# Optimization experiments

Measured on AMD Instinct MI355X. Metric: run time of the kernel, lower is better.

The kernel has to match this reference:

```python
import jax, jax.numpy as jnp
import numpy as np
from jax import lax

# Model dims (from init_kwargs / mamba_ssm defaults)
D_MODEL = 256
EXPAND = 2
D_INNER = EXPAND * D_MODEL      # 512
D_STATE = 64                     # ssm_rank
DT_RANK = D_MODEL // 16          # 16 (mamba_ssm default ceil(d_model/16))
D_CONV = 4
IMG = 384
PATCH = 16
BATCH = 16
NUM_CLASSES = 10
NBLK = 6                         # sum(depths) = 2+2+2
GRID = IMG // PATCH
NTOK = GRID * GRID + 1           # 577 (patches + cls token)


def setup_inputs() -> dict:
    key = jax.random.key(0)
    ks = iter(jax.random.split(key, 32))
    rn = lambda shape, s=0.02: jax.random.normal(next(ks), shape, jnp.float32) * s
    inp = {}
    inp["x"] = jax.random.normal(next(ks), (BATCH, 3, IMG, IMG), jnp.float32)
    # patch embed conv
    inp["patch_w"] = rn((D_MODEL, 3, PATCH, PATCH), 0.05)
    inp["patch_b"] = jnp.zeros((D_MODEL,), jnp.float32)
    inp["cls_token"] = rn((1, 1, D_MODEL))
    inp["pos_embed"] = rn((1, NTOK, D_MODEL))
    # stacked per-block Mamba params
    inp["norm_w"] = jnp.ones((NBLK, D_MODEL), jnp.float32)
    inp["norm_b"] = jnp.zeros((NBLK, D_MODEL), jnp.float32)
    inp["in_proj_w"] = rn((NBLK, 2 * D_INNER, D_MODEL))
    inp["conv_w"] = rn((NBLK, D_INNER, 1, D_CONV), 0.1)
    inp["conv_b"] = jnp.zeros((NBLK, D_INNER), jnp.float32)
    inp["x_proj_w"] = rn((NBLK, DT_RANK + 2 * D_STATE, D_INNER))
    inp["dt_proj_w"] = rn((NBLK, D_INNER, DT_RANK), 0.1)
    inp["dt_proj_b"] = rn((NBLK, D_INNER), 0.5)
    # S4D-real init: A = -[1..d_state]
    inp["A_log"] = jnp.log(jnp.broadcast_to(
        jnp.arange(1, D_STATE + 1, dtype=jnp.float32), (NBLK, D_INNER, D_STATE)))
    inp["D_ssm"] = jnp.ones((NBLK, D_INNER), jnp.float32)
    inp["out_proj_w"] = rn((NBLK, D_MODEL, D_INNER))
    inp["fnorm_w"] = jnp.ones((D_MODEL,), jnp.float32)
    inp["fnorm_b"] = jnp.zeros((D_MODEL,), jnp.float32)
    inp["head_w"] = rn((NUM_CLASSES, D_MODEL))
    inp["head_b"] = jnp.zeros((NUM_CLASSES,), jnp.float32)
    return inp


def layer_norm(x, w, b, eps=1e-5):
    mu = jnp.mean(x, axis=-1, keepdims=True)
    var = jnp.mean(jnp.square(x - mu), axis=-1, keepdims=True)
    return (x - mu) * lax.rsqrt(var + eps) * w + b


def causal_dwconv(x, w, b):
    # x: (B, di, L), w: (di, 1, K) depthwise; causal left pad K-1
    K = w.shape[-1]
    y = lax.conv_general_dilated(x, w, (1,), [(K - 1, 0)],
                                 dimension_numbers=("NCH", "OIH", "NCH"),
                                 feature_group_count=x.shape[1])
    return y + b[None, :, None]


def selective_scan(u, dt, A, Bm, Cm, Dp):
    # u, dt: (B, L, di); Bm, Cm: (B, L, ds); A: (di, ds); Dp: (di,)
    def step(h, inp):
        dt_t, B_t, C_t, u_t = inp                       # (B,di),(B,ds),(B,ds),(B,di)
        dA = jnp.exp(dt_t[:, :, None] * A)              # (B, di, ds)
        h = dA * h + (dt_t * u_t)[:, :, None] * B_t[:, None, :]
        y = jnp.einsum('bds,bs->bd', h, C_t)
        return h, y
    h0 = jnp.zeros((u.shape[0], A.shape[0], A.shape[1]), u.dtype)
    _, ys = lax.scan(step, h0, (dt.transpose(1, 0, 2), Bm.transpose(1, 0, 2),
                                Cm.transpose(1, 0, 2), u.transpose(1, 0, 2)))
    return ys.transpose(1, 0, 2) + u * Dp


def mamba_block(x, nw, nb, inw, cw, cb, xpw, dtw, dtb, alog, dp, ow):
    res = x
    x = layer_norm(x, nw, nb)
    xz = jnp.einsum('bld,ed->ble', x, inw)              # (B, L, 2*di)
    xi, z = jnp.split(xz, 2, axis=-1)
    xi = causal_dwconv(xi.transpose(0, 2, 1), cw, cb).transpose(0, 2, 1)
    xi = jax.nn.silu(xi)
    dbl = jnp.einsum('bld,ed->ble', xi, xpw)            # (B, L, dt_rank + 2*ds)
    dtr = dbl[..., :DT_RANK]
    Bm = dbl[..., DT_RANK:DT_RANK + D_STATE]
    Cm = dbl[..., DT_RANK + D_STATE:]
    dt = jax.nn.softplus(jnp.einsum('blr,dr->bld', dtr, dtw) + dtb)
    A = -jnp.exp(alog)
    y = selective_scan(xi, dt, A, Bm, Cm, dp)
    y = y * jax.nn.silu(z)
    return res + jnp.einsum('bld,ed->ble', y, ow)


def reference(x, patch_w, patch_b, cls_token, pos_embed,
              norm_w, norm_b, in_proj_w, conv_w, conv_b, x_proj_w,
              dt_proj_w, dt_proj_b, A_log, D_ssm, out_proj_w,
              fnorm_w, fnorm_b, head_w, head_b):
    B = x.shape[0]
    h = lax.conv_general_dilated(x, patch_w, (PATCH, PATCH), 'VALID',
                                 dimension_numbers=("NCHW", "OIHW", "NCHW"))
    h = h + patch_b[None, :, None, None]
    h = h.reshape(B, D_MODEL, -1).transpose(0, 2, 1)    # (B, G*G, D)
    h = jnp.concatenate([jnp.broadcast_to(cls_token, (B, 1, D_MODEL)), h], axis=1)
    h = h + pos_embed
    for i in range(NBLK):
        h = mamba_block(h, norm_w[i], norm_b[i], in_proj_w[i], conv_w[i], conv_b[i],
                        x_proj_w[i], dt_proj_w[i], dt_proj_b[i], A_log[i], D_ssm[i],
                        out_proj_w[i])
    h = layer_norm(h, fnorm_w, fnorm_b)
    return h[:, 0] @ head_w.T + head_b
```

## Files before the change

kernel.cpp:

```cpp
#include <hip/hip_runtime.h>
#include <hip/hip_bf16.h>
#include <cstdint>
#include <cstddef>

#define L_TOK 577
#define DM 256
#define DI 512
#define DS_ 64
#define NROWS (16*577)
#define PROWS (16*576)
#define NCH 37

typedef float f32x4v __attribute__((ext_vector_type(4)));
typedef __bf16 bf16x8 __attribute__((ext_vector_type(8)));

__device__ __forceinline__ float fast_exp2(float x) {
#if __has_builtin(__builtin_amdgcn_exp2f)
    return __builtin_amdgcn_exp2f(x);
#else
    return __expf(x * 0.6931471805599453f);
#endif
}

__global__ __launch_bounds__(256)
void k_gemm(const float* __restrict__ A, int lda,
            const float* __restrict__ B, int ldb,
            float* __restrict__ C, int ldc,
            int M, int N, int K, int beta)
{
    __shared__ char sA[128*64*2];
    __shared__ char sB[128*64*2];
    const int tid  = threadIdx.x;
    const int lane = tid & 63;
    const int wave = tid >> 6;
    const int wr = wave >> 1, wc = wave & 1;
    const int tm = blockIdx.y * 128, tn = blockIdx.x * 128;

    f32x4v acc[4][4];
#pragma unroll
    for (int m = 0; m < 4; ++m)
#pragma unroll
        for (int n = 0; n < 4; ++n) acc[m][n] = (f32x4v){0.f, 0.f, 0.f, 0.f};

    const int nk = K >> 6;
    for (int kt = 0; kt < nk; ++kt) {
        const int k0 = kt << 6;
        __syncthreads();
#pragma unroll
        for (int i = 0; i < 4; ++i) {
            int c = tid + (i << 8);
            int row = c >> 3, slot = c & 7;
            int gr = tm + row; gr = gr < M ? gr : M - 1;
            const float* src = A + (size_t)gr * lda + k0 + (slot << 3);
            float4 lo = *reinterpret_cast<const float4*>(src);
            float4 hi = *reinterpret_cast<const float4*>(src + 4);
            bf16x8 pk;
            pk[0]=(__bf16)lo.x; pk[1]=(__bf16)lo.y; pk[2]=(__bf16)lo.z; pk[3]=(__bf16)lo.w;
            pk[4]=(__bf16)hi.x; pk[5]=(__bf16)hi.y; pk[6]=(__bf16)hi.z; pk[7]=(__bf16)hi.w;
            *reinterpret_cast<bf16x8*>(&sA[(row << 7) + ((slot ^ (row & 7)) << 4)]) = pk;
        }
#pragma unroll
        for (int i = 0; i < 4; ++i) {
            int c = tid + (i << 8);
            int row = c >> 3, slot = c & 7;
            int gr = tn + row; gr = gr < N ? gr : N - 1;
            const float* src = B + (size_t)gr * ldb + k0 + (slot << 3);
            float4 lo = *reinterpret_cast<const float4*>(src);
            float4 hi = *reinterpret_cast<const float4*>(src + 4);
            bf16x8 pk;
            pk[0]=(__bf16)lo.x; pk[1]=(__bf16)lo.y; pk[2]=(__bf16)lo.z; pk[3]=(__bf16)lo.w;
            pk[4]=(__bf16)hi.x; pk[5]=(__bf16)hi.y; pk[6]=(__bf16)hi.z; pk[7]=(__bf16)hi.w;
            *reinterpret_cast<bf16x8*>(&sB[(row << 7) + ((slot ^ (row & 7)) << 4)]) = pk;
        }
        __syncthreads();

        bf16x8 af[4][2], bfr[4][2];
#pragma unroll
        for (int kk = 0; kk < 2; ++kk) {
            int sl = (kk << 2) + (lane >> 4);
#pragma unroll
            for (int m = 0; m < 4; ++m) {
                int row = (wr << 6) + (m << 4) + (lane & 15);
                af[m][kk] = *reinterpret_cast<const bf16x8*>(&sA[(row << 7) + ((sl ^ (row & 7)) << 4)]);
            }
#pragma unroll
            for (int n = 0; n < 4; ++n) {
                int row = (wc << 6) + (n << 4) + (lane & 15);
                bfr[n][kk] = *reinterpret_cast<const bf16x8*>(&sB[(row << 7) + ((sl ^ (row & 7)) << 4)]);
            }
        }
#pragma unroll
        for (int kk = 0; kk < 2; ++kk)
#pragma unroll
            for (int m = 0; m < 4; ++m)
#pragma unroll
                for (int n = 0; n < 4; ++n)
                    acc[m][n] = __builtin_amdgcn_mfma_f32_16x16x32_bf16(af[m][kk], bfr[n][kk], acc[m][n], 0, 0, 0);
    }

#pragma unroll
    for (int m = 0; m < 4; ++m) {
        int grow0 = tm + (wr << 6) + (m << 4) + ((lane >> 4) << 2);
#pragma unroll
        for (int n = 0; n < 4; ++n) {
            int gcol = tn + (wc << 6) + (n << 4) + (lane & 15);
            if (gcol < N) {
#pragma unroll
                for (int j = 0; j < 4; ++j) {
                    int grow = grow0 + j;
                    if (grow < M) {
                        size_t o = (size_t)grow * ldc + gcol;
                        float v = acc[m][n][j];
                        if (beta) v += C[o];
                        C[o] = v;
                    }
                }
            }
        }
    }
}

__global__ __launch_bounds__(256)
void k_im2col(const float* __restrict__ x, float* __restrict__ xcol)
{
    int id = blockIdx.x * 256 + threadIdx.x;
    int kh = id & 15;
    int ci = (id >> 4) % 3;
    int row = id / 48;
    int b = row / 576, p = row % 576;
    int py = p / 24, px = p % 24;
    const float* src = x + ((size_t)(b*3 + ci)*384 + py*16 + kh)*384 + px*16;
    float* dst = xcol + (size_t)row*768 + ci*256 + kh*16;
#pragma unroll
    for (int j = 0; j < 4; ++j)
        *reinterpret_cast<float4*>(dst + j*4) = *reinterpret_cast<const float4*>(src + j*4);
}

__global__ __launch_bounds__(256)
void k_assemble(const float* __restrict__ Ctmp, const float* __restrict__ pb,
                const float* __restrict__ cls, const float* __restrict__ pos,
                float* __restrict__ h_tok)
{
    int i4 = blockIdx.x * 256 + threadIdx.x;
    int c4 = i4 & 63;
    int tok = (i4 >> 6) % 577;
    int b = i4 / (577*64);
    float4 pv = *reinterpret_cast<const float4*>(pos + tok*256 + c4*4);
    float4 r;
    if (tok == 0) {
        float4 cv = *reinterpret_cast<const float4*>(cls + c4*4);
        r.x = cv.x + pv.x; r.y = cv.y + pv.y; r.z = cv.z + pv.z; r.w = cv.w + pv.w;
    } else {
        float4 t = *reinterpret_cast<const float4*>(Ctmp + (size_t)(b*576 + tok - 1)*256 + c4*4);
        float4 bb = *reinterpret_cast<const float4*>(pb + c4*4);
        r.x = t.x + bb.x + pv.x; r.y = t.y + bb.y + pv.y;
        r.z = t.z + bb.z + pv.z; r.w = t.w + bb.w + pv.w;
    }
    *reinterpret_cast<float4*>(h_tok + (size_t)i4*4) = r;
}

__global__ __launch_bounds__(256)
void k_ln(const float* __restrict__ X, const float* __restrict__ w,
          const float* __restrict__ bb, float* __restrict__ O)
{
    int lane = threadIdx.x & 63;
    int row = blockIdx.x * 4 + (threadIdx.x >> 6);
    const float4 v = *reinterpret_cast<const float4*>(X + (size_t)row*256 + lane*4);
    float s1 = v.x + v.y + v.z + v.w;
    float s2 = v.x*v.x + v.y*v.y + v.z*v.z + v.w*v.w;
#pragma unroll
    for (int o2 = 32; o2; o2 >>= 1) { s1 += __shfl_xor(s1, o2); s2 += __shfl_xor(s2, o2); }
    float mu = s1 * (1.f/256.f);
    float var = s2 * (1.f/256.f) - mu*mu;
    float rs = rsqrtf(var + 1e-5f);
    float4 wv = *reinterpret_cast<const float4*>(w + lane*4);
    float4 bv = *reinterpret_cast<const float4*>(bb + lane*4);
    float4 o;
    o.x = (v.x - mu)*rs*wv.x + bv.x;
    o.y = (v.y - mu)*rs*wv.y + bv.y;
    o.z = (v.z - mu)*rs*wv.z + bv.z;
    o.w = (v.w - mu)*rs*wv.w + bv.w;
    *reinterpret_cast<float4*>(O + (size_t)row*256 + lane*4) = o;
}

__global__ __launch_bounds__(256)
void k_conv(const float* __restrict__ xz, const float* __restrict__ cw,
            const float* __restrict__ cb, float* __restrict__ xi)
{
    int gw = blockIdx.x * 4 + (threadIdx.x >> 6);
    int lane = threadIdx.x & 63;
    int tc = gw % 73;
    int eg = (gw / 73) & 7;
    int b  = gw / (73*8);
    int e = eg*64 + lane;
    float4 wv = *reinterpret_cast<const float4*>(cw + e*4);
    float bias = cb[e];
    int t0 = tc * 8;
    float xv[11];
#pragma unroll
    for (int j = 0; j < 11; ++j) {
        int t = t0 - 3 + j;
        xv[j] = (t >= 0 && t < 577) ? xz[(size_t)(b*577 + t)*1024 + e] : 0.f;
    }
#pragma unroll
    for (int j = 0; j < 8; ++j) {
        int t = t0 + j;
        if (t < 577) {
            float a = wv.x*xv[j] + wv.y*xv[j+1] + wv.z*xv[j+2] + wv.w*xv[j+3] + bias;
            float sgm = 1.f / (1.f + __expf(-a));
            xi[(size_t)(b*577 + t)*512 + e] = a * sgm;
        }
    }
}

__global__ __launch_bounds__(256)
void k_dtfuse(const float* __restrict__ dbl, const float* __restrict__ dtw,
              const float* __restrict__ dtb, const float* __restrict__ xi,
              float* __restrict__ tri2)
{
    __shared__ float dtr[16][16];
    const int tid = threadIdx.x;
    const int b    = blockIdx.x / 74;
    const int rr   = blockIdx.x % 74;
    const int tc   = rr >> 1;
    const int e    = ((rr & 1) << 8) + tid;
    const int nj   = (tc == 36) ? 1 : 16;
    {
        int j = tid >> 4, r = tid & 15;
        if (tid < 256 && j < nj)
            dtr[j][r] = dbl[((size_t)(b*577) + tc*16 + j)*144 + r];
    }
    __syncthreads();
    const float* wp = dtw + e*16;
    float4 w0 = *reinterpret_cast<const float4*>(wp);
    float4 w1 = *reinterpret_cast<const float4*>(wp + 4);
    float4 w2 = *reinterpret_cast<const float4*>(wp + 8);
    float4 w3 = *reinterpret_cast<const float4*>(wp + 12);
    float bias = dtb[e];
    float* outp = tri2 + ((size_t)(b*37 + tc)*512 + e)*32;
    for (int j = 0; j < nj; ++j) {
        const float* dr = dtr[j];
        float accv = bias;
        accv += w0.x*dr[0] + w0.y*dr[1] + w0.z*dr[2] + w0.w*dr[3];
        accv += w1.x*dr[4] + w1.y*dr[5] + w1.z*dr[6] + w1.w*dr[7];
        accv += w2.x*dr[8] + w2.y*dr[9] + w2.z*dr[10] + w2.w*dr[11];
        accv += w3.x*dr[12] + w3.y*dr[13] + w3.z*dr[14] + w3.w*dr[15];
        float sp = accv > 20.f ? accv : log1pf(__expf(accv));
        float u = xi[((size_t)(b*577) + tc*16 + j)*512 + e];
        float2 o; o.x = sp; o.y = sp * u;
        *reinterpret_cast<float2*>(outp + j*2) = o;
    }
}

__global__ __launch_bounds__(256, 6)
void k_scan(const float* __restrict__ tri2, const float* __restrict__ dbl,
            const float* __restrict__ A_log, float* __restrict__ y)
{
    __shared__ float tp[4*16*65];
    const int tid  = threadIdx.x;
    const int lane = tid & 63;
    const int wv   = tid >> 6;
    const int bb   = blockIdx.x >> 7;
    const int d    = __builtin_amdgcn_readfirstlane(((blockIdx.x & 127) << 2) + wv);
    const float alog2 = -__expf(A_log[(size_t)d*64 + lane]) * 1.44269504f;
    const float2* trp = reinterpret_cast<const float2*>(tri2)
                      + ((size_t)bb*NCH*512 + d)*16;
    const float* Bb = dbl + (size_t)bb*577*144 + 16 + lane;
    float* yp = y + (size_t)bb*577*512 + d;
    float* tpw = tp + wv*(16*65);
    const int g = lane >> 4, tt = lane & 15;
    float h = 0.f;

    for (int c = 0; c < 36; ++c) {
        const int t0 = c << 4;
        float p[16];
#pragma unroll
        for (int j = 0; j < 16; ++j) {
            float2 tr = trp[(size_t)c*8192 + j];
            float Bv = Bb[(size_t)(t0 + j)*144];
            float Cv = Bb[(size_t)(t0 + j)*144 + 64];
            float dA = fast_exp2(tr.x * alog2);
            h = __builtin_fmaf(dA, h, tr.y * Bv);
            p[j] = h * Cv;
        }
#pragma unroll
        for (int j = 0; j < 16; ++j) tpw[j*65 + lane] = p[j];
        float partial = 0.f;
        {
            const float* rp = tpw + tt*65 + g*16;
#pragma unroll
            for (int k = 0; k < 16; ++k) partial += rp[k];
        }
        partial += __shfl_xor(partial, 16);
        partial += __shfl_xor(partial, 32);
        if (lane < 16) yp[(size_t)(t0 + tt)*512] = partial;
    }
    {
        float2 tr = trp[(size_t)36*8192];
        float Bv = Bb[(size_t)576*144];
        float Cv = Bb[(size_t)576*144 + 64];
        float dA = fast_exp2(tr.x * alog2);
        h = __builtin_fmaf(dA, h, tr.y * Bv);
        float p = h * Cv;
        p += __shfl_xor(p, 32); p += __shfl_xor(p, 16); p += __shfl_xor(p, 8);
        p += __shfl_xor(p, 4);  p += __shfl_xor(p, 2);  p += __shfl_xor(p, 1);
        if (lane == 0) yp[(size_t)576*512] = p;
    }
}

__global__ __launch_bounds__(256)
void k_gate(float* __restrict__ y, const float* __restrict__ xz,
            const float* __restrict__ xi, const float* __restrict__ Dp)
{
    int i4 = blockIdx.x * 256 + threadIdx.x;
    int row = i4 >> 7;
    int c4 = i4 & 127;
    float4 yv = *reinterpret_cast<float4*>(y + (size_t)i4*4);
    float4 uv = *reinterpret_cast<const float4*>(xi + (size_t)i4*4);
    float4 dv = *reinterpret_cast<const float4*>(Dp + c4*4);
    const float4 zv = *reinterpret_cast<const float4*>(xz + (size_t)row*1024 + 512 + c4*4);
    float4 o;
    o.x = (yv.x + uv.x*dv.x) * (zv.x / (1.f + __expf(-zv.x)));
    o.y = (yv.y + uv.y*dv.y) * (zv.y / (1.f + __expf(-zv.y)));
    o.z = (yv.z + uv.z*dv.z) * (zv.z / (1.f + __expf(-zv.z)));
    o.w = (yv.w + uv.w*dv.w) * (zv.w / (1.f + __expf(-zv.w)));
    *reinterpret_cast<float4*>(y + (size_t)i4*4) = o;
}

__global__ __launch_bounds__(256)
void k_head(const float* __restrict__ h_tok, const float* __restrict__ fw,
            const float* __restrict__ fb, const float* __restrict__ hw,
            const float* __restrict__ hb, float* __restrict__ out)
{
    int b = blockIdx.x, tid = threadIdx.x;
    __shared__ float sv[256];
    __shared__ float sr[16];
    float v = h_tok[(size_t)b*577*256 + tid];
    float s1 = v, s2 = v*v;
#pragma unroll
    for (int o2 = 32; o2; o2 >>= 1) { s1 += __shfl_xor(s1, o2); s2 += __shfl_xor(s2, o2); }
    int wave = tid >> 6;
    if ((tid & 63) == 0) { sr[wave] = s1; sr[wave + 8] = s2; }
    __syncthreads();
    float t1 = sr[0] + sr[1] + sr[2] + sr[3];
    float t2 = sr[8] + sr[9] + sr[10] + sr[11];
    float mu = t1 * (1.f/256.f);
    float var = t2 * (1.f/256.f) - mu*mu;
    float rs = rsqrtf(var + 1e-5f);
    sv[tid] = (v - mu)*rs*fw[tid] + fb[tid];
    __syncthreads();
    if (tid < 10) {
        float acc = hb[tid];
        for (int d2 = 0; d2 < 256; ++d2) acc += sv[d2]*hw[tid*256 + d2];
        out[b*10 + tid] = acc;
    }
}

extern "C" void kernel_launch(void* const* d_in, const int* in_sizes, int n_in,
                              void* d_out, int out_size, void* d_ws, size_t ws_size,
                              hipStream_t stream)
{
    const float* x         = (const float*)d_in[0];
    const float* patch_w   = (const float*)d_in[1];
    const float* patch_b   = (const float*)d_in[2];
    const float* cls_tok   = (const float*)d_in[3];
    const float* pos_emb   = (const float*)d_in[4];
    const float* norm_w    = (const float*)d_in[5];
    const float* norm_b    = (const float*)d_in[6];
    const float* in_proj_w = (const float*)d_in[7];
    const float* conv_w    = (const float*)d_in[8];
    const float* conv_b    = (const float*)d_in[9];
    const float* x_proj_w  = (const float*)d_in[10];
    const float* dt_proj_w = (const float*)d_in[11];
    const float* dt_proj_b = (const float*)d_in[12];
    const float* A_log     = (const float*)d_in[13];
    const float* D_ssm     = (const float*)d_in[14];
    const float* out_proj_w= (const float*)d_in[15];
    const float* fnorm_w   = (const float*)d_in[16];
    const float* fnorm_b   = (const float*)d_in[17];
    const float* head_w    = (const float*)d_in[18];
    const float* head_b    = (const float*)d_in[19];
    float* out = (float*)d_out;

    char* ws = (char*)d_ws;
    size_t off = 0;
    auto carve = [&](size_t bytes) -> float* {
        float* p = (float*)(ws + off);
        off += (bytes + 255) & ~(size_t)255;
        return p;
    };
    float* h_tok = carve((size_t)NROWS*DM*4);
    float* xln   = carve((size_t)NROWS*DM*4);
    float* xz    = carve((size_t)NROWS*1024*4);
    float* xi    = carve((size_t)NROWS*DI*4);
    float* dbl   = carve((size_t)NROWS*144*4);
    float* tri2  = carve((size_t)16*NCH*DI*32*4);
    float* yb    = carve((size_t)NROWS*DI*4);
    float* xcol  = xz;
    float* Ctmp  = xi;

    k_im2col<<<1728, 256, 0, stream>>>(x, xcol);
    {
        dim3 g(2, 72);
        k_gemm<<<g, 256, 0, stream>>>(xcol, 768, patch_w, 768, Ctmp, 256, PROWS, 256, 768, 0);
    }
    k_assemble<<<2308, 256, 0, stream>>>(Ctmp, patch_b, cls_tok, pos_emb, h_tok);

    for (int i = 0; i < 6; ++i) {
        k_ln<<<2308, 256, 0, stream>>>(h_tok, norm_w + i*DM, norm_b + i*DM, xln);
        {
            dim3 g(8, 73);
            k_gemm<<<g, 256, 0, stream>>>(xln, DM, in_proj_w + (size_t)i*1024*DM, DM,
                                          xz, 1024, NROWS, 1024, DM, 0);
        }
        k_conv<<<2336, 256, 0, stream>>>(xz, conv_w + (size_t)i*DI*4, conv_b + i*DI, xi);
        {
            dim3 g(2, 73);
            k_gemm<<<g, 256, 0, stream>>>(xi, DI, x_proj_w + (size_t)i*144*DI, DI,
                                          dbl, 144, NROWS, 144, DI, 0);
        }
        k_dtfuse<<<16*NCH*2, 256, 0, stream>>>(dbl, dt_proj_w + (size_t)i*DI*16, dt_proj_b + i*DI,
                                               xi, tri2);
        k_scan<<<2048, 256, 0, stream>>>(tri2, dbl, A_log + (size_t)i*DI*DS_, yb);
        k_gate<<<4616, 256, 0, stream>>>(yb, xz, xi, D_ssm + i*DI);
        {
            dim3 g(2, 73);
            k_gemm<<<g, 256, 0, stream>>>(yb, DI, out_proj_w + (size_t)i*DM*DI, DI,
                                          h_tok, DM, NROWS, DM, DI, 1);
        }
    }
    k_head<<<16, 256, 0, stream>>>(h_tok, fnorm_w, fnorm_b, head_w, head_b, out);
}
```

Baseline: 1.846 ms.

## Store intermediates and weights in bf16, scan two channels per wave with chunked output

Intermediate activations (xln, xz, xi, yb, im2col) are now stored as bf16 instead of fp32. Weights are pre-converted to bf16 with a new conversion kernel, so the GEMM loads bf16 directly without converting in the load loop. The scan kernel now processes two channels per wave and writes a chunked [b, chunk, d, 16] layout, which the gate kernel reads back. The intent is to halve memory traffic and increase per-wave work, at the cost of some precision and an extra weight-conversion pass on every call.

New measurement: 1.694 ms. 8.2% less time.

```diff
diff --git a/kernel.cpp b/kernel.cpp
--- a/kernel.cpp
+++ b/kernel.cpp
@@ -13,6 +13,7 @@
 
 typedef float f32x4v __attribute__((ext_vector_type(4)));
 typedef __bf16 bf16x8 __attribute__((ext_vector_type(8)));
+typedef __bf16 bf16x4 __attribute__((ext_vector_type(4)));
 
 __device__ __forceinline__ float fast_exp2(float x) {
 #if __has_builtin(__builtin_amdgcn_exp2f)
@@ -22,14 +23,27 @@
 #endif
 }
 
-__global__ __launch_bounds__(256)
-void k_gemm(const float* __restrict__ A, int lda,
-            const float* __restrict__ B, int ldb,
-            float* __restrict__ C, int ldc,
-            int M, int N, int K, int beta)
-{
-    __shared__ char sA[128*64*2];
-    __shared__ char sB[128*64*2];
+__device__ __forceinline__ bf16x4 to_bf4(float a, float b, float c, float d) {
+    bf16x4 r; r[0]=(__bf16)a; r[1]=(__bf16)b; r[2]=(__bf16)c; r[3]=(__bf16)d; return r;
+}
+
+__global__ __launch_bounds__(256)
+void k_cvt(const float* __restrict__ s, __bf16* __restrict__ d, int n4)
+{
+    for (int i = blockIdx.x*256 + threadIdx.x; i < n4; i += gridDim.x*256) {
+        float4 v = *reinterpret_cast<const float4*>(s + (size_t)i*4);
+        *reinterpret_cast<bf16x4*>(d + (size_t)i*4) = to_bf4(v.x, v.y, v.z, v.w);
+    }
+}
+
+__global__ __launch_bounds__(256)
+void k_gemm(const __bf16* __restrict__ A, int lda,
+            const __bf16* __restrict__ B, int ldb,
+            void* __restrict__ Cvp, int ldc,
+            int M, int N, int K, int cmode)
+{
+    __shared__ char sA[128*128];
+    __shared__ char sB[128*128];
     const int tid  = threadIdx.x;
     const int lane = tid & 63;
     const int wave = tid >> 6;
@@ -51,26 +65,16 @@
             int c = tid + (i << 8);
             int row = c >> 3, slot = c & 7;
             int gr = tm + row; gr = gr < M ? gr : M - 1;
-            const float* src = A + (size_t)gr * lda + k0 + (slot << 3);
-            float4 lo = *reinterpret_cast<const float4*>(src);
-            float4 hi = *reinterpret_cast<const float4*>(src + 4);
-            bf16x8 pk;
-            pk[0]=(__bf16)lo.x; pk[1]=(__bf16)lo.y; pk[2]=(__bf16)lo.z; pk[3]=(__bf16)lo.w;
-            pk[4]=(__bf16)hi.x; pk[5]=(__bf16)hi.y; pk[6]=(__bf16)hi.z; pk[7]=(__bf16)hi.w;
-            *reinterpret_cast<bf16x8*>(&sA[(row << 7) + ((slot ^ (row & 7)) << 4)]) = pk;
+            bf16x8 va = *reinterpret_cast<const bf16x8*>(A + (size_t)gr*lda + k0 + (slot<<3));
+            *reinterpret_cast<bf16x8*>(&sA[(row << 7) + ((slot ^ (row & 7)) << 4)]) = va;
         }
 #pragma unroll
         for (int i = 0; i < 4; ++i) {
             int c = tid + (i << 8);
             int row = c >> 3, slot = c & 7;
             int gr = tn + row; gr = gr < N ? gr : N - 1;
-            const float* src = B + (size_t)gr * ldb + k0 + (slot << 3);
-            float4 lo = *reinterpret_cast<const float4*>(src);
-            float4 hi = *reinterpret_cast<const float4*>(src + 4);
-            bf16x8 pk;
-            pk[0]=(__bf16)lo.x; pk[1]=(__bf16)lo.y; pk[2]=(__bf16)lo.z; pk[3]=(__bf16)lo.w;
-            pk[4]=(__bf16)hi.x; pk[5]=(__bf16)hi.y; pk[6]=(__bf16)hi.z; pk[7]=(__bf16)hi.w;
-            *reinterpret_cast<bf16x8*>(&sB[(row << 7) + ((slot ^ (row & 7)) << 4)]) = pk;
+            bf16x8 vb = *reinterpret_cast<const bf16x8*>(B + (size_t)gr*ldb + k0 + (slot<<3));
+            *reinterpret_cast<bf16x8*>(&sB[(row << 7) + ((slot ^ (row & 7)) << 4)]) = vb;
         }
         __syncthreads();
 
@@ -98,6 +102,8 @@
                     acc[m][n] = __builtin_amdgcn_mfma_f32_16x16x32_bf16(af[m][kk], bfr[n][kk], acc[m][n], 0, 0, 0);
     }
 
+    float* Cf = (float*)Cvp;
+    __bf16* Ch = (__bf16*)Cvp;
 #pragma unroll
     for (int m = 0; m < 4; ++m) {
         int grow0 = tm + (wr << 6) + (m << 4) + ((lane >> 4) << 2);
@@ -111,8 +117,9 @@
                     if (grow < M) {
                         size_t o = (size_t)grow * ldc + gcol;
                         float v = acc[m][n][j];
-                        if (beta) v += C[o];
-                        C[o] = v;
+                        if (cmode == 1)      Cf[o] = v + Cf[o];
+                        else if (cmode == 2) Ch[o] = (__bf16)v;
+                        else                 Cf[o] = v;
                     }
                 }
             }
@@ -121,7 +128,7 @@
 }
 
 __global__ __launch_bounds__(256)
-void k_im2col(const float* __restrict__ x, float* __restrict__ xcol)
+void k_im2col(const float* __restrict__ x, __bf16* __restrict__ xcol)
 {
     int id = blockIdx.x * 256 + threadIdx.x;
     int kh = id & 15;
@@ -130,10 +137,12 @@
     int b = row / 576, p = row % 576;
     int py = p / 24, px = p % 24;
     const float* src = x + ((size_t)(b*3 + ci)*384 + py*16 + kh)*384 + px*16;
-    float* dst = xcol + (size_t)row*768 + ci*256 + kh*16;
-#pragma unroll
-    for (int j = 0; j < 4; ++j)
-        *reinterpret_cast<float4*>(dst + j*4) = *reinterpret_cast<const float4*>(src + j*4);
+    __bf16* dst = xcol + (size_t)row*768 + ci*256 + kh*16;
+#pragma unroll
+    for (int j = 0; j < 4; ++j) {
+        float4 v = *reinterpret_cast<const float4*>(src + j*4);
+        *reinterpret_cast<bf16x4*>(dst + j*4) = to_bf4(v.x, v.y, v.z, v.w);
+    }
 }
 
 __global__ __launch_bounds__(256)
@@ -161,7 +170,7 @@
 
 __global__ __launch_bounds__(256)
 void k_ln(const float* __restrict__ X, const float* __restrict__ w,
-          const float* __restrict__ bb, float* __restrict__ O)
+          const float* __restrict__ bb, __bf16* __restrict__ O)
 {
     int lane = threadIdx.x & 63;
     int row = blockIdx.x * 4 + (threadIdx.x >> 6);
@@ -175,17 +184,14 @@
     float rs = rsqrtf(var + 1e-5f);
     float4 wv = *reinterpret_cast<const float4*>(w + lane*4);
     float4 bv = *reinterpret_cast<const float4*>(bb + lane*4);
-    float4 o;
-    o.x = (v.x - mu)*rs*wv.x + bv.x;
-    o.y = (v.y - mu)*rs*wv.y + bv.y;
-    o.z = (v.z - mu)*rs*wv.z + bv.z;
-    o.w = (v.w - mu)*rs*wv.w + bv.w;
-    *reinterpret_cast<float4*>(O + (size_t)row*256 + lane*4) = o;
-}
-
-__global__ __launch_bounds__(256)
-void k_conv(const float* __restrict__ xz, const float* __restrict__ cw,
-            const float* __restrict__ cb, float* __restrict__ xi)
+    *reinterpret_cast<bf16x4*>(O + (size_t)row*256 + lane*4) =
+        to_bf4((v.x - mu)*rs*wv.x + bv.x, (v.y - mu)*rs*wv.y + bv.y,
+               (v.z - mu)*rs*wv.z + bv.z, (v.w - mu)*rs*wv.w + bv.w);
+}
+
+__global__ __launch_bounds__(256)
+void k_conv(const __bf16* __restrict__ xz, const float* __restrict__ cw,
+            const float* __restrict__ cb, __bf16* __restrict__ xi)
 {
     int gw = blockIdx.x * 4 + (threadIdx.x >> 6);
     int lane = threadIdx.x & 63;
@@ -200,7 +206,7 @@
 #pragma unroll
     for (int j = 0; j < 11; ++j) {
         int t = t0 - 3 + j;
-        xv[j] = (t >= 0 && t < 577) ? xz[(size_t)(b*577 + t)*1024 + e] : 0.f;
+        xv[j] = (t >= 0 && t < 577) ? (float)xz[(size_t)(b*577 + t)*1024 + e] : 0.f;
     }
 #pragma unroll
     for (int j = 0; j < 8; ++j) {
@@ -208,14 +214,14 @@
         if (t < 577) {
             float a = wv.x*xv[j] + wv.y*xv[j+1] + wv.z*xv[j+2] + wv.w*xv[j+3] + bias;
             float sgm = 1.f / (1.f + __expf(-a));
-            xi[(size_t)(b*577 + t)*512 + e] = a * sgm;
+            xi[(size_t)(b*577 + t)*512 + e] = (__bf16)(a * sgm);
         }
     }
 }
 
 __global__ __launch_bounds__(256)
 void k_dtfuse(const float* __restrict__ dbl, const float* __restrict__ dtw,
-              const float* __restrict__ dtb, const float* __restrict__ xi,
+              const float* __restrict__ dtb, const __bf16* __restrict__ xi,
               float* __restrict__ tri2)
 {
     __shared__ float dtr[16][16];
@@ -227,7 +233,7 @@
     const int nj   = (tc == 36) ? 1 : 16;
     {
         int j = tid >> 4, r = tid & 15;
-        if (tid < 256 && j < nj)
+        if (j < nj)
             dtr[j][r] = dbl[((size_t)(b*577) + tc*16 + j)*144 + r];
     }
     __syncthreads();
@@ -246,85 +252,106 @@
         accv += w2.x*dr[8] + w2.y*dr[9] + w2.z*dr[10] + w2.w*dr[11];
         accv += w3.x*dr[12] + w3.y*dr[13] + w3.z*dr[14] + w3.w*dr[15];
         float sp = accv > 20.f ? accv : log1pf(__expf(accv));
-        float u = xi[((size_t)(b*577) + tc*16 + j)*512 + e];
+        float u = (float)xi[((size_t)(b*577) + tc*16 + j)*512 + e];
         float2 o; o.x = sp; o.y = sp * u;
         *reinterpret_cast<float2*>(outp + j*2) = o;
     }
 }
 
-__global__ __launch_bounds__(256, 6)
+__global__ __launch_bounds__(256, 4)
 void k_scan(const float* __restrict__ tri2, const float* __restrict__ dbl,
-            const float* __restrict__ A_log, float* __restrict__ y)
+            const float* __restrict__ A_log, float* __restrict__ ych)
 {
     __shared__ float tp[4*16*65];
     const int tid  = threadIdx.x;
     const int lane = tid & 63;
     const int wv   = tid >> 6;
-    const int bb   = blockIdx.x >> 7;
-    const int d    = __builtin_amdgcn_readfirstlane(((blockIdx.x & 127) << 2) + wv);
-    const float alog2 = -__expf(A_log[(size_t)d*64 + lane]) * 1.44269504f;
+    const int bb   = blockIdx.x >> 6;
+    const int d0   = __builtin_amdgcn_readfirstlane(((blockIdx.x & 63) << 3) + (wv << 1));
+    const float al0 = -__expf(A_log[(size_t)d0*64 + lane]) * 1.44269504f;
+    const float al1 = -__expf(A_log[(size_t)(d0+1)*64 + lane]) * 1.44269504f;
     const float2* trp = reinterpret_cast<const float2*>(tri2)
-                      + ((size_t)bb*NCH*512 + d)*16;
+                      + ((size_t)bb*NCH*512 + d0)*16;
     const float* Bb = dbl + (size_t)bb*577*144 + 16 + lane;
-    float* yp = y + (size_t)bb*577*512 + d;
+    float* yo = ych + ((size_t)bb*NCH*512 + d0)*16;
     float* tpw = tp + wv*(16*65);
     const int g = lane >> 4, tt = lane & 15;
-    float h = 0.f;
+    float h0 = 0.f, h1 = 0.f;
 
     for (int c = 0; c < 36; ++c) {
         const int t0 = c << 4;
-        float p[16];
+        float p0[16], p1[16];
 #pragma unroll
         for (int j = 0; j < 16; ++j) {
-            float2 tr = trp[(size_t)c*8192 + j];
+            float2 u0 = trp[(size_t)c*8192 + j];
+            float2 u1 = trp[(size_t)c*8192 + 16 + j];
             float Bv = Bb[(size_t)(t0 + j)*144];
             float Cv = Bb[(size_t)(t0 + j)*144 + 64];
-            float dA = fast_exp2(tr.x * alog2);
-            h = __builtin_fmaf(dA, h, tr.y * Bv);
-            p[j] = h * Cv;
-        }
-#pragma unroll
-        for (int j = 0; j < 16; ++j) tpw[j*65 + lane] = p[j];
-        float partial = 0.f;
+            h0 = __builtin_fmaf(fast_exp2(u0.x*al0), h0, u0.y*Bv);
+            h1 = __builtin_fmaf(fast_exp2(u1.x*al1), h1, u1.y*Bv);
+            p0[j] = h0 * Cv;
+            p1[j] = h1 * Cv;
+        }
+#pragma unroll
+        for (int j = 0; j < 16; ++j) tpw[j*65 + lane] = p0[j];
+        float s0 = 0.f;
         {
             const float* rp = tpw + tt*65 + g*16;
 #pragma unroll
-            for (int k = 0; k < 16; ++k) partial += rp[k];
-        }
-        partial += __shfl_xor(partial, 16);
-        partial += __shfl_xor(partial, 32);
-        if (lane < 16) yp[(size_t)(t0 + tt)*512] = partial;
+            for (int k = 0; k < 16; ++k) s0 += rp[k];
+        }
+        s0 += __shfl_xor(s0, 16); s0 += __shfl_xor(s0, 32);
+        if (lane < 16) yo[(size_t)c*8192 + tt] = s0;
+#pragma unroll
+        for (int j = 0; j < 16; ++j) tpw[j*65 + lane] = p1[j];
+        float s1 = 0.f;
+        {
+            const float* rp = tpw + tt*65 + g*16;
+#pragma unroll
+            for (int k = 0; k < 16; ++k) s1 += rp[k];
+        }
+        s1 += __shfl_xor(s1, 16); s1 += __shfl_xor(s1, 32);
+        if (lane < 16) yo[(size_t)c*8192 + 16 + tt] = s1;
     }
     {
-        float2 tr = trp[(size_t)36*8192];
+        float2 u0 = trp[(size_t)36*8192];
+        float2 u1 = trp[(size_t)36*8192 + 16];
         float Bv = Bb[(size_t)576*144];
         float Cv = Bb[(size_t)576*144 + 64];
-        float dA = fast_exp2(tr.x * alog2);
-        h = __builtin_fmaf(dA, h, tr.y * Bv);
-        float p = h * Cv;
-        p += __shfl_xor(p, 32); p += __shfl_xor(p, 16); p += __shfl_xor(p, 8);
-        p += __shfl_xor(p, 4);  p += __shfl_xor(p, 2);  p += __shfl_xor(p, 1);
-        if (lane == 0) yp[(size_t)576*512] = p;
-    }
-}
-
-__global__ __launch_bounds__(256)
-void k_gate(float* __restrict__ y, const float* __restrict__ xz,
-            const float* __restrict__ xi, const float* __restrict__ Dp)
+        h0 = __builtin_fmaf(fast_exp2(u0.x*al0), h0, u0.y*Bv);
+        h1 = __builtin_fmaf(fast_exp2(u1.x*al1), h1, u1.y*Bv);
+        float q0 = h0 * Cv, q1 = h1 * Cv;
+#pragma unroll
+        for (int o2 = 32; o2; o2 >>= 1) { q0 += __shfl_xor(q0, o2); q1 += __shfl_xor(q1, o2); }
+        if (lane == 0) {
+            yo[(size_t)36*8192] = q0;
+            yo[(size_t)36*8192 + 16] = q1;
+        }
+    }
+}
+
+__global__ __launch_bounds__(256)
+void k_gate(const float* __restrict__ ych, const __bf16* __restrict__ xz,
+            const __bf16* __restrict__ xi, const float* __restrict__ Dp,
+            __bf16* __restrict__ yb)
 {
     int i4 = blockIdx.x * 256 + threadIdx.x;
     int row = i4 >> 7;
     int c4 = i4 & 127;
-    float4 yv = *reinterpret_cast<float4*>(y + (size_t)i4*4);
-    float4 uv = *reinterpret_cast<const float4*>(xi + (size_t)i4*4);
-    float4 dv = *reinterpret_cast<const float4*>(Dp + c4*4);
-    const float4 zv = *reinterpret_cast<const float4*>(xz + (size_t)row*1024 + 512 + c4*4);
-    float4 o;
-    o.x = (yv.x + uv.x*dv.x) * (zv.x / (1.f + __expf(-zv.x)));
-    o.y = (yv.y + uv.y*dv.y) * (zv.y / (1.f + __expf(-zv.y)));
-    o.z = (yv.z + uv.z*dv.z) * (zv.z / (1.f + __expf(-zv.z)));
-    o.w = (yv.w + uv.w*dv.w) * (zv.w / (1.f + __expf(-zv.w)));
-    *reinterpret_cast<float4*>(y + (size_t)i4*4) = o;
+    int b = row / 577, t = row % 577;
+    int cc = t >> 4, tt = t & 15;
+    int d = c4 << 2;
+    const float* yp = ych + ((size_t)(b*NCH + cc)*512 + d)*16 + tt;
+    float y0 = yp[0], y1 = yp[16], y2 = yp[32], y3 = yp[48];
+    bf16x4 u4 = *reinterpret_cast<const bf16x4*>(xi + (size_t)row*512 + d);
+    bf16x4 z4 = *reinterpret_cast<const bf16x4*>(xz + (size_t)row*1024 + 512 + d);
+    float4 dv = *reinterpret_cast<const float4*>(Dp + d);
+    float z0 = (float)z4[0], z1 = (float)z4[1], z2 = (float)z4[2], z3 = (float)z4[3];
+    float g0 = z0 / (1.f + __expf(-z0)), g1 = z1 / (1.f + __expf(-z1));
+    float g2 = z2 / (1.f + __expf(-z2)), g3 = z3 / (1.f + __expf(-z3));
+    *reinterpret_cast<bf16x4*>(yb + (size_t)row*512 + d) =
+        to_bf4((y0 + (float)u4[0]*dv.x) * g0, (y1 + (float)u4[1]*dv.y) * g1,
+               (y2 + (float)u4[2]*dv.z) * g2, (y3 + (float)u4[3]*dv.w) * g3);
 }
 
 __global__ __launch_bounds__(256)
@@ -384,25 +411,35 @@
 
     char* ws = (char*)d_ws;
     size_t off = 0;
-    auto carve = [&](size_t bytes) -> float* {
-        float* p = (float*)(ws + off);
+    auto carveB = [&](size_t bytes) -> char* {
+        char* p = ws + off;
         off += (bytes + 255) & ~(size_t)255;
         return p;
     };
-    float* h_tok = carve((size_t)NROWS*DM*4);
-    float* xln   = carve((size_t)NROWS*DM*4);
-    float* xz    = carve((size_t)NROWS*1024*4);
-    float* xi    = carve((size_t)NROWS*DI*4);
-    float* dbl   = carve((size_t)NROWS*144*4);
-    float* tri2  = carve((size_t)16*NCH*DI*32*4);
-    float* yb    = carve((size_t)NROWS*DI*4);
-    float* xcol  = xz;
-    float* Ctmp  = xi;
+    float*  h_tok = (float*) carveB((size_t)NROWS*DM*4);
+    __bf16* xln   = (__bf16*)carveB((size_t)NROWS*DM*2);
+    __bf16* xz    = (__bf16*)carveB((size_t)NROWS*1024*2);
+    __bf16* xi    = (__bf16*)carveB((size_t)NROWS*DI*2);
+    float*  dbl   = (float*) carveB((size_t)NROWS*144*4);
+    float*  tri2  = (float*) carveB((size_t)16*NCH*DI*32*4);
+    float*  ych   = (float*) carveB((size_t)16*NCH*DI*16*4);
+    __bf16* yb    = (__bf16*)carveB((size_t)NROWS*DI*2);
+    __bf16* pwb   = (__bf16*)carveB((size_t)196608*2);
+    __bf16* iwb   = (__bf16*)carveB((size_t)6*1024*DM*2);
+    __bf16* xwb   = (__bf16*)carveB((size_t)6*144*DI*2);
+    __bf16* owb   = (__bf16*)carveB((size_t)6*DM*DI*2);
+    __bf16* xcol  = xz;
+    float*  Ctmp  = ych;
+
+    k_cvt<<<192, 256, 0, stream>>>(patch_w, pwb, 196608/4);
+    k_cvt<<<1024, 256, 0, stream>>>(in_proj_w, iwb, (6*1024*DM)/4);
+    k_cvt<<<432, 256, 0, stream>>>(x_proj_w, xwb, (6*144*DI)/4);
+    k_cvt<<<768, 256, 0, stream>>>(out_proj_w, owb, (6*DM*DI)/4);
 
     k_im2col<<<1728, 256, 0, stream>>>(x, xcol);
     {
         dim3 g(2, 72);
-        k_gemm<<<g, 256, 0, stream>>>(xcol, 768, patch_w, 768, Ctmp, 256, PROWS, 256, 768, 0);
+        k_gemm<<<g, 256, 0, stream>>>(xcol, 768, pwb, 768, Ctmp, 256, PROWS, 256, 768, 0);
     }
     k_assemble<<<2308, 256, 0, stream>>>(Ctmp, patch_b, cls_tok, pos_emb, h_tok);
 
@@ -410,22 +447,22 @@
         k_ln<<<2308, 256, 0, stream>>>(h_tok, norm_w + i*DM, norm_b + i*DM, xln);
         {
             dim3 g(8, 73);
-            k_gemm<<<g, 256, 0, stream>>>(xln, DM, in_proj_w + (size_t)i*1024*DM, DM,
-                                          xz, 1024, NROWS, 1024, DM, 0);
+            k_gemm<<<g, 256, 0, stream>>>(xln, DM, iwb + (size_t)i*1024*DM, DM,
+                                          xz, 1024, NROWS, 1024, DM, 2);
         }
         k_conv<<<2336, 256, 0, stream>>>(xz, conv_w + (size_t)i*DI*4, conv_b + i*DI, xi);
         {
             dim3 g(2, 73);
-            k_gemm<<<g, 256, 0, stream>>>(xi, DI, x_proj_w + (size_t)i*144*DI, DI,
+            k_gemm<<<g, 256, 0, stream>>>(xi, DI, xwb + (size_t)i*144*DI, DI,
                                           dbl, 144, NROWS, 144, DI, 0);
         }
         k_dtfuse<<<16*NCH*2, 256, 0, stream>>>(dbl, dt_proj_w + (size_t)i*DI*16, dt_proj_b + i*DI,
                                                xi, tri2);
-        k_scan<<<2048, 256, 0, stream>>>(tri2, dbl, A_log + (size_t)i*DI*DS_, yb);
-        k_gate<<<4616, 256, 0, stream>>>(yb, xz, xi, D_ssm + i*DI);
+        k_scan<<<1024, 256, 0, stream>>>(tri2, dbl, A_log + (size_t)i*DI*DS_, ych);
+        k_gate<<<4616, 256, 0, stream>>>(ych, xz, xi, D_ssm + i*DI, yb);
         {
             dim3 g(2, 73);
-            k_gemm<<<g, 256, 0, stream>>>(yb, DI, out_proj_w + (size_t)i*DM*DI, DI,
+            k_gemm<<<g, 256, 0, stream>>>(yb, DI, owb + (size_t)i*DM*DI, DI,
                                           h_tok, DM, NROWS, DM, DI, 1);
         }
     }
```
